# Performance work log

Measured on AMD Instinct MI355X. Metric: run time of the kernel, lower is better.

## Reference

```python
import jax, jax.numpy as jnp
import numpy as np

B, V, F, P = 32, 256, 128, 64

def setup_inputs() -> dict:
    key = jax.random.key(0)
    k1, k2, k3, k4, k5 = jax.random.split(key, 5)
    q2_obs_scaled = jax.random.uniform(k1, (B, P), dtype=jnp.float32) * 3.0
    amplitude_logits = jax.random.normal(k2, (B, 1, F, P), dtype=jnp.float32)
    volumes = jax.random.uniform(k3, (V, 1), dtype=jnp.float32) + 0.5  # NonNeg, ~median 1
    filters = jax.random.uniform(k4, (1, F), dtype=jnp.float32) * 3.0  # NonNeg q2 positions
    sigma = jax.random.uniform(k5, (), dtype=jnp.float32) * 0.025 + 0.015  # in [0.015, 0.04]
    return {"q2_obs_scaled": q2_obs_scaled, "amplitude_logits": amplitude_logits,
            "volumes": volumes, "filters": filters, "sigma": sigma}

def reference(q2_obs_scaled, amplitude_logits, volumes, filters, sigma):
    # q2_filters: (V,1)*(1,F) -> (V,F) -> (1,V,F,1)
    q2_filters = (volumes * filters)[None, :, :, None]
    # q2_obs_scaled: (B,P) -> (B,1,1,P); difference: (B,V,F,P)
    difference = q2_filters - q2_obs_scaled[:, None, None, :]
    amplitudes = jax.nn.softmax(amplitude_logits, axis=3)  # (B,1,F,P)
    inv = 1.0 / (sigma + 0.001)
    distances = amplitudes * jnp.exp(-0.5 * (difference * inv) ** 2)
    metric = jnp.sum(distances, axis=3)  # (B,V,F)
    return metric
```

## Files before the change

### kernel.cpp

```cpp
#include <hip/hip_runtime.h>

#define B 32
#define V 256
#define F 128
#define P 64

#define LOG2E 1.44269504088896340736f

__global__ __launch_bounds__(256) void extraction_kernel(
    const float* __restrict__ q2,
    const float* __restrict__ logits,
    const float* __restrict__ vol,
    const float* __restrict__ filt,
    const float* __restrict__ sigma_p,
    float* __restrict__ out)
{
    const int bid = blockIdx.x;
    const int b   = bid >> 7;
    const int f   = bid & (F - 1);
    const int tid = threadIdx.x;

    __shared__ float q_s[P];
    __shared__ float amp_s[P];

    if (tid < P) {
        float l = logits[bid * P + tid];
        float m = l;
        #pragma unroll
        for (int off = 32; off > 0; off >>= 1)
            m = fmaxf(m, __shfl_xor(m, off, 64));
        float e = __builtin_amdgcn_exp2f((l - m) * LOG2E);
        float s = e;
        #pragma unroll
        for (int off = 32; off > 0; off >>= 1)
            s += __shfl_xor(s, off, 64);
        amp_s[tid] = e / s;
        q_s[tid]   = q2[b * P + tid];
    }
    __syncthreads();

    const float sig = sigma_p[0];
    const float inv = 1.0f / (sig + 0.001f);
    const float kk  = -0.5f * LOG2E * inv * inv;

    const float x = vol[tid] * filt[f];

    float acc0 = 0.f, acc1 = 0.f, acc2 = 0.f, acc3 = 0.f;
    const float4* q4 = (const float4*)q_s;
    const float4* a4 = (const float4*)amp_s;
    #pragma unroll
    for (int j = 0; j < P / 4; ++j) {
        float4 qv = q4[j];
        float4 av = a4[j];
        float d0 = x - qv.x;
        float d1 = x - qv.y;
        float d2 = x - qv.z;
        float d3 = x - qv.w;
        acc0 += av.x * __builtin_amdgcn_exp2f(kk * d0 * d0);
        acc1 += av.y * __builtin_amdgcn_exp2f(kk * d1 * d1);
        acc2 += av.z * __builtin_amdgcn_exp2f(kk * d2 * d2);
        acc3 += av.w * __builtin_amdgcn_exp2f(kk * d3 * d3);
    }

    out[(b * V + tid) * F + f] = (acc0 + acc1) + (acc2 + acc3);
}

extern "C" void kernel_launch(void* const* d_in, const int* in_sizes, int n_in,
                              void* d_out, int out_size, void* d_ws, size_t ws_size,
                              hipStream_t stream) {
    const float* q2     = (const float*)d_in[0];
    const float* logits = (const float*)d_in[1];
    const float* vol    = (const float*)d_in[2];
    const float* filt   = (const float*)d_in[3];
    const float* sigma  = (const float*)d_in[4];
    float* out = (float*)d_out;

    extraction_kernel<<<B * F, V, 0, stream>>>(q2, logits, vol, filt, sigma, out);
}
```

Before: 76.17 us.

## Split softmax into separate kernel and remap threads to coalesce output stores

Moves the softmax into a standalone kernel that writes amplitudes to workspace. The main kernel now maps threads to f instead of v, so output stores along f are coalesced rather than strided by F. Each thread keeps its amplitude row in registers and loops over a tile of v values, with q read uniformly from global memory. This costs a second launch, a workspace round trip and higher register pressure (64 floats per thread).

```diff
diff --git a/kernel.cpp b/kernel.cpp
--- a/kernel.cpp
+++ b/kernel.cpp
@@ -6,63 +6,72 @@
 #define P 64
 
 #define LOG2E 1.44269504088896340736f
+#define VTILE 8
+
+__global__ __launch_bounds__(256) void softmax_kernel(
+    const float* __restrict__ logits,
+    float* __restrict__ amp)
+{
+    const int bf = blockIdx.x * 4 + (threadIdx.x >> 6);
+    const int p  = threadIdx.x & 63;
+
+    float l = logits[bf * P + p];
+    float m = l;
+    #pragma unroll
+    for (int off = 32; off > 0; off >>= 1)
+        m = fmaxf(m, __shfl_xor(m, off, 64));
+    float e = __builtin_amdgcn_exp2f((l - m) * LOG2E);
+    float s = e;
+    #pragma unroll
+    for (int off = 32; off > 0; off >>= 1)
+        s += __shfl_xor(s, off, 64);
+    amp[bf * P + p] = e / s;
+}
 
 __global__ __launch_bounds__(256) void extraction_kernel(
     const float* __restrict__ q2,
-    const float* __restrict__ logits,
+    const float* __restrict__ amp,
     const float* __restrict__ vol,
     const float* __restrict__ filt,
     const float* __restrict__ sigma_p,
     float* __restrict__ out)
 {
-    const int bid = blockIdx.x;
-    const int b   = bid >> 7;
-    const int f   = bid & (F - 1);
-    const int tid = threadIdx.x;
-
-    __shared__ float q_s[P];
-    __shared__ float amp_s[P];
-
-    if (tid < P) {
-        float l = logits[bid * P + tid];
-        float m = l;
-        #pragma unroll
-        for (int off = 32; off > 0; off >>= 1)
-            m = fmaxf(m, __shfl_xor(m, off, 64));
-        float e = __builtin_amdgcn_exp2f((l - m) * LOG2E);
-        float s = e;
-        #pragma unroll
-        for (int off = 32; off > 0; off >>= 1)
-            s += __shfl_xor(s, off, 64);
-        amp_s[tid] = e / s;
-        q_s[tid]   = q2[b * P + tid];
-    }
-    __syncthreads();
+    const int b  = blockIdx.x >> 5;
+    const int v0 = (blockIdx.x & 31) * VTILE;
+    const int f  = threadIdx.x & (F - 1);
+    const int vh = threadIdx.x >> 7;
 
     const float sig = sigma_p[0];
     const float inv = 1.0f / (sig + 0.001f);
     const float kk  = -0.5f * LOG2E * inv * inv;
+    const float ff  = filt[f];
 
-    const float x = vol[tid] * filt[f];
+    float4 a[P / 4];
+    const float4* __restrict__ arow = (const float4*)(amp + (b * F + f) * P);
+    #pragma unroll
+    for (int j = 0; j < P / 4; ++j) a[j] = arow[j];
 
-    float acc0 = 0.f, acc1 = 0.f, acc2 = 0.f, acc3 = 0.f;
-    const float4* q4 = (const float4*)q_s;
-    const float4* a4 = (const float4*)amp_s;
+    const float4* __restrict__ qrow = (const float4*)(q2 + b * P);
+
     #pragma unroll
-    for (int j = 0; j < P / 4; ++j) {
-        float4 qv = q4[j];
-        float4 av = a4[j];
-        float d0 = x - qv.x;
-        float d1 = x - qv.y;
-        float d2 = x - qv.z;
-        float d3 = x - qv.w;
-        acc0 += av.x * __builtin_amdgcn_exp2f(kk * d0 * d0);
-        acc1 += av.y * __builtin_amdgcn_exp2f(kk * d1 * d1);
-        acc2 += av.z * __builtin_amdgcn_exp2f(kk * d2 * d2);
-        acc3 += av.w * __builtin_amdgcn_exp2f(kk * d3 * d3);
+    for (int vi = vh; vi < VTILE; vi += 2) {
+        const int v   = v0 + vi;
+        const float x = vol[v] * ff;
+        float acc0 = 0.f, acc1 = 0.f, acc2 = 0.f, acc3 = 0.f;
+        #pragma unroll
+        for (int j = 0; j < P / 4; ++j) {
+            float4 qv = qrow[j];
+            float d0 = x - qv.x;
+            float d1 = x - qv.y;
+            float d2 = x - qv.z;
+            float d3 = x - qv.w;
+            acc0 += a[j].x * __builtin_amdgcn_exp2f(kk * d0 * d0);
+            acc1 += a[j].y * __builtin_amdgcn_exp2f(kk * d1 * d1);
+            acc2 += a[j].z * __builtin_amdgcn_exp2f(kk * d2 * d2);
+            acc3 += a[j].w * __builtin_amdgcn_exp2f(kk * d3 * d3);
+        }
+        out[(b * V + v) * F + f] = (acc0 + acc1) + (acc2 + acc3);
     }
-
-    out[(b * V + tid) * F + f] = (acc0 + acc1) + (acc2 + acc3);
 }
 
 extern "C" void kernel_launch(void* const* d_in, const int* in_sizes, int n_in,
@@ -74,6 +83,8 @@
     const float* filt   = (const float*)d_in[3];
     const float* sigma  = (const float*)d_in[4];
     float* out = (float*)d_out;
+    float* amp = (float*)d_ws;
 
-    extraction_kernel<<<B * F, V, 0, stream>>>(q2, logits, vol, filt, sigma, out);
+    softmax_kernel<<<B * F / 4, 256, 0, stream>>>(logits, amp);
+    extraction_kernel<<<B * (V / VTILE), 256, 0, stream>>>(q2, amp, vol, filt, sigma, out);
 }
```

Measured after the change: 79.82 us. 4.8% more time.

## Remap blocks to batch×volume tiles so threads span filters and stores coalesce

Applied to the files above, without the earlier changes.

Blocks now cover one batch and a tile of 16 volumes, with threads indexed by filter instead of volume. This makes the output writes contiguous along F rather than strided by F. Each block computes the softmax for all F rows of its batch into a padded LDS array. Each thread then keeps its amplitude row and the q2 row in registers and loops over volumes. Softmax no longer subtracts the row max, and it is recomputed redundantly across the 16 blocks of each batch. The grid shrinks to 512 blocks, which reduces parallelism, and the float4 LDS reads from 65-float rows are not 16-byte aligned.

```diff
diff --git a/kernel.cpp b/kernel.cpp
--- a/kernel.cpp
+++ b/kernel.cpp
@@ -4,7 +4,8 @@
 #define V 256
 #define F 128
 #define P 64
-
+#define VTILE 16
+#define LDSROW 65
 #define LOG2E 1.44269504088896340736f
 
 __global__ __launch_bounds__(256) void extraction_kernel(
@@ -15,54 +16,65 @@
     const float* __restrict__ sigma_p,
     float* __restrict__ out)
 {
-    const int bid = blockIdx.x;
-    const int b   = bid >> 7;
-    const int f   = bid & (F - 1);
+    const int b   = blockIdx.x >> 4;
+    const int v0  = (blockIdx.x & 15) * VTILE;
     const int tid = threadIdx.x;
 
-    __shared__ float q_s[P];
-    __shared__ float amp_s[P];
+    __shared__ float amp_s[F * LDSROW];
 
-    if (tid < P) {
-        float l = logits[bid * P + tid];
-        float m = l;
+    {
+        const int wave = tid >> 6;
+        const int lane = tid & 63;
         #pragma unroll
-        for (int off = 32; off > 0; off >>= 1)
-            m = fmaxf(m, __shfl_xor(m, off, 64));
-        float e = __builtin_amdgcn_exp2f((l - m) * LOG2E);
-        float s = e;
-        #pragma unroll
-        for (int off = 32; off > 0; off >>= 1)
-            s += __shfl_xor(s, off, 64);
-        amp_s[tid] = e / s;
-        q_s[tid]   = q2[b * P + tid];
+        for (int r = 0; r < F / 4; ++r) {
+            const int f = wave * (F / 4) + r;
+            float l = logits[(b * F + f) * P + lane];
+            float e = __builtin_amdgcn_exp2f(l * LOG2E);
+            float s = e;
+            #pragma unroll
+            for (int off = 32; off > 0; off >>= 1)
+                s += __shfl_xor(s, off, 64);
+            amp_s[f * LDSROW + lane] = e / s;
+        }
     }
     __syncthreads();
+
+    const int f  = tid & (F - 1);
+    const int vh = tid >> 7;
 
     const float sig = sigma_p[0];
     const float inv = 1.0f / (sig + 0.001f);
     const float kk  = -0.5f * LOG2E * inv * inv;
+    const float ffv = filt[f];
 
-    const float x = vol[tid] * filt[f];
+    float4 a[P / 4];
+    #pragma unroll
+    for (int j = 0; j < P / 4; ++j)
+        a[j] = *(const float4*)&amp_s[f * LDSROW + j * 4];
 
-    float acc0 = 0.f, acc1 = 0.f, acc2 = 0.f, acc3 = 0.f;
-    const float4* q4 = (const float4*)q_s;
-    const float4* a4 = (const float4*)amp_s;
+    float4 q[P / 4];
+    const float4* __restrict__ qrow = (const float4*)(q2 + b * P);
     #pragma unroll
-    for (int j = 0; j < P / 4; ++j) {
-        float4 qv = q4[j];
-        float4 av = a4[j];
-        float d0 = x - qv.x;
-        float d1 = x - qv.y;
-        float d2 = x - qv.z;
-        float d3 = x - qv.w;
-        acc0 += av.x * __builtin_amdgcn_exp2f(kk * d0 * d0);
-        acc1 += av.y * __builtin_amdgcn_exp2f(kk * d1 * d1);
-        acc2 += av.z * __builtin_amdgcn_exp2f(kk * d2 * d2);
-        acc3 += av.w * __builtin_amdgcn_exp2f(kk * d3 * d3);
+    for (int j = 0; j < P / 4; ++j) q[j] = qrow[j];
+
+    #pragma unroll 2
+    for (int vi = 0; vi < VTILE / 2; ++vi) {
+        const int v   = v0 + vi * 2 + vh;
+        const float x = vol[v] * ffv;
+        float acc0 = 0.f, acc1 = 0.f, acc2 = 0.f, acc3 = 0.f;
+        #pragma unroll
+        for (int j = 0; j < P / 4; ++j) {
+            float d0 = x - q[j].x;
+            float d1 = x - q[j].y;
+            float d2 = x - q[j].z;
+            float d3 = x - q[j].w;
+            acc0 += a[j].x * __builtin_amdgcn_exp2f((kk * d0) * d0);
+            acc1 += a[j].y * __builtin_amdgcn_exp2f((kk * d1) * d1);
+            acc2 += a[j].z * __builtin_amdgcn_exp2f((kk * d2) * d2);
+            acc3 += a[j].w * __builtin_amdgcn_exp2f((kk * d3) * d3);
+        }
+        out[(b * V + v) * F + f] = (acc0 + acc1) + (acc2 + acc3);
     }
-
-    out[(b * V + tid) * F + f] = (acc0 + acc1) + (acc2 + acc3);
 }
 
 extern "C" void kernel_launch(void* const* d_in, const int* in_sizes, int n_in,
@@ -75,5 +87,5 @@
     const float* sigma  = (const float*)d_in[4];
     float* out = (float*)d_out;
 
-    extraction_kernel<<<B * F, V, 0, stream>>>(q2, logits, vol, filt, sigma, out);
+    extraction_kernel<<<B * (V / VTILE), 256, 0, stream>>>(q2, logits, vol, filt, sigma, out);
 }
```

Measured after the change: 79.30 us. 4.1% more time.
